# Kernel tuning notes

Measured on AMD Instinct MI355X. Metric: run time of the kernel, lower is better.

## Reference

```python
import jax, jax.numpy as jnp
import numpy as np

B, T, D, A = 8, 256, 512, 512  # hidden dim D must equal attn size A per the TF code


def setup_inputs() -> dict:
    key = jax.random.key(0)
    ks = jax.random.split(key, 12)
    g = lambda k, shp, fan: jax.random.normal(k, shp, jnp.float32) * (1.0 / np.sqrt(fan))
    return {
        "state_outputs": jax.random.normal(ks[0], (B, T, D), jnp.float32),
        "final_state": jax.random.normal(ks[1], (B, D), jnp.float32),
        "intent_v": g(ks[2], (A,), A),
        "W_ih": g(ks[3], (D, A), D), "b_ih": jnp.zeros((A,), jnp.float32),
        "W_ii": g(ks[4], (D, A), D), "b_ii": jnp.zeros((A,), jnp.float32),
        "slot_v": g(ks[5], (A,), A),
        "W_sh": g(ks[6], (D, A), D), "b_sh": jnp.zeros((A,), jnp.float32),
        "W_si": g(ks[7], (D, A), D), "b_si": jnp.zeros((A,), jnp.float32),
    }


def reference(state_outputs, final_state, intent_v, W_ih, b_ih, W_ii, b_ii,
              slot_v, W_sh, b_sh, W_si, b_si):
    # ---- intent attention ----
    ih = jnp.einsum('btd,da->bta', state_outputs, W_ih) + b_ih        # [B,T,A]
    ii = final_state @ W_ii + b_ii                                     # [B,A]
    intent_score = jnp.sum(intent_v * jnp.tanh(ih + ii[:, None, :]), axis=-1)  # [B,T]
    intent_w = jax.nn.softmax(intent_score, axis=-1)
    c_intent = jnp.einsum('bt,btd->bd', intent_w, state_outputs)       # [B,D]

    # ---- slot attention ----
    sh = jnp.einsum('btd,da->bta', state_outputs, W_sh) + b_sh         # keys   [B,T,A]
    si = jnp.einsum('btd,da->bta', state_outputs, W_si) + b_si         # queries[B,T,A]
    # score[b,t,s] over pairs: tanh(sh[b,s] + si[b,t]) . slot_v
    slot_score = jnp.sum(slot_v * jnp.tanh(sh[:, None, :, :] + si[:, :, None, :]), axis=-1)  # [B,T,T]
    slot_w = jax.nn.softmax(slot_score, axis=-1)
    c_slot = jnp.einsum('bts,bsd->btd', slot_w, state_outputs)         # [B,T,D]
    return c_slot, c_intent
```

## Files before the change

kernel.cpp:

```cpp
#include <hip/hip_runtime.h>

#define BB 8
#define TT 256
#define DD 512
#define AA 512

#define PS 2.8853900817779268f
#define LOG2E 1.4426950408889634f

typedef __attribute__((ext_vector_type(8))) short short8;
typedef __attribute__((ext_vector_type(4))) float f32x4;

__device__ __forceinline__ float fast_tanh(float x) {
    float e = __builtin_amdgcn_exp2f(x * PS);
    float r = __builtin_amdgcn_rcpf(1.0f + e);
    return fmaf(-2.0f, r, 1.0f);
}

__device__ __forceinline__ ushort f2bf(float x) {
    uint u = __float_as_uint(x);
    uint r = (u + 0x7fffu + ((u >> 16) & 1u)) >> 16;
    return (ushort)r;
}
__device__ __forceinline__ float bf2f(ushort h) {
    return __uint_as_float(((uint)h) << 16);
}

__global__ __launch_bounds__(256) void prep(const float* __restrict__ SO,
                                            ushort* __restrict__ Ast,
                                            const float* __restrict__ Wsh,
                                            const float* __restrict__ Wsi,
                                            const float* __restrict__ Wih,
                                            ushort* __restrict__ Wt,
                                            const float* __restrict__ fs_g,
                                            const float* __restrict__ Wii,
                                            const float* __restrict__ bii,
                                            float* __restrict__ ii) {
    const int bid = blockIdx.x;
    const int tid = threadIdx.x;
    __shared__ float T[32][33];
    __shared__ float fs[DD];

    if (bid < 16) {
        int b = bid >> 1, half = bid & 1;
        int a = half * 256 + tid;
        fs[tid]       = fs_g[b * DD + tid];
        fs[tid + 256] = fs_g[b * DD + tid + 256];
        __syncthreads();
        float acc = bii[a];
        #pragma unroll 8
        for (int d = 0; d < DD; ++d)
            acc = fmaf(fs[d], Wii[(size_t)d * AA + a], acc);
        ii[b * AA + a] = acc;
    } else if (bid < 784) {
        int lbid = bid - 16;
        int z = lbid >> 8;
        int rem = lbid & 255;
        const float* W = (z == 0) ? Wsh : (z == 1) ? Wsi : Wih;
        int k0 = (rem & 15) * 32, n0 = (rem >> 4) * 32;
        int tx = tid & 31, ty = tid >> 5;
        #pragma unroll
        for (int r = 0; r < 4; ++r) {
            int kl = ty * 4 + r;
            T[kl][tx] = W[(size_t)(k0 + kl) * 512 + n0 + tx];
        }
        __syncthreads();
        size_t nbase = (size_t)z * 512 + n0;
        #pragma unroll
        for (int r = 0; r < 4; ++r) {
            int nl = ty * 4 + r;
            float v = T[tx][nl];
            ushort hi = f2bf(v);
            ushort lo = f2bf(v - bf2f(hi));
            Wt[(nbase + nl) * 1024 + k0 + tx]       = hi;
            Wt[(nbase + nl) * 1024 + 512 + k0 + tx] = lo;
        }
    } else {
        int qid = (bid - 784) * 256 + tid;
        int m = qid >> 7;
        int k4 = (qid & 127) * 4;
        float4 v = *reinterpret_cast<const float4*>(&SO[(size_t)m * 512 + k4]);
        ushort4 hi, lo;
        hi.x = f2bf(v.x); lo.x = f2bf(v.x - bf2f(hi.x));
        hi.y = f2bf(v.y); lo.y = f2bf(v.y - bf2f(hi.y));
        hi.z = f2bf(v.z); lo.z = f2bf(v.z - bf2f(hi.z));
        hi.w = f2bf(v.w); lo.w = f2bf(v.w - bf2f(hi.w));
        *reinterpret_cast<ushort4*>(&Ast[(size_t)m * 1024 + k4])       = hi;
        *reinterpret_cast<ushort4*>(&Ast[(size_t)m * 1024 + 512 + k4]) = lo;
    }
}

__global__ __launch_bounds__(256) void gemm_mfma(
    const ushort* __restrict__ Ast, const ushort* __restrict__ Wt,
    const float* __restrict__ bsh, const float* __restrict__ bsi,
    const float* __restrict__ bih,
    const float* __restrict__ ii, const float* __restrict__ iv,
    float* __restrict__ EhT, float* __restrict__ Es, float* __restrict__ ipart) {
    __shared__ ushort Al[64 * 64];
    __shared__ ushort Bl[64 * 64];
    const int tid = threadIdx.x;
    const int wave = tid >> 6, lane = tid & 63;
    const int wr = wave >> 1, wc = wave & 1;
    const int m0 = blockIdx.x * 64;
    const int by = blockIdx.y;
    const int n0 = by * 64;
    const int r8 = lane >> 3, c8 = lane & 7;
    const int l15 = lane & 15, kb = lane >> 4;

    f32x4 acc[2][2] = {};

    const char* Ab = reinterpret_cast<const char*>(Ast);
    const char* Bb = reinterpret_cast<const char*>(Wt);
    char* AlB = reinterpret_cast<char*>(Al);
    char* BlB = reinterpret_cast<char*>(Bl);

    for (int k0 = 0; k0 < 1536; k0 += 64) {
        int abyte = (k0 < 1024 ? k0 : k0 - 1024) * 2;
        int bbyte = (k0 < 512 ? k0 : k0 - 512) * 2;
        #pragma unroll
        for (int inst = 0; inst < 2; ++inst) {
            int row = wave * 16 + inst * 8 + r8;
            short8 av = *reinterpret_cast<const short8*>(
                Ab + (size_t)(m0 + row) * 2048 + abyte + c8 * 16);
            *reinterpret_cast<short8*>(AlB + row * 128 + ((c8 ^ r8) * 16)) = av;
            short8 bv = *reinterpret_cast<const short8*>(
                Bb + (size_t)(n0 + row) * 2048 + bbyte + c8 * 16);
            *reinterpret_cast<short8*>(BlB + row * 128 + ((c8 ^ r8) * 16)) = bv;
        }
        __syncthreads();
        #pragma unroll
        for (int kk = 0; kk < 2; ++kk) {
            short8 af[2], bf[2];
            #pragma unroll
            for (int i = 0; i < 2; ++i) {
                int ra = wr * 32 + i * 16 + l15;
                int sa = (kk * 4 + kb) ^ (ra & 7);
                af[i] = *reinterpret_cast<const short8*>(AlB + ra * 128 + sa * 16);
                int rb = wc * 32 + i * 16 + l15;
                int sbx = (kk * 4 + kb) ^ (rb & 7);
                bf[i] = *reinterpret_cast<const short8*>(BlB + rb * 128 + sbx * 16);
            }
            #pragma unroll
            for (int i = 0; i < 2; ++i)
                #pragma unroll
                for (int j = 0; j < 2; ++j)
                    acc[i][j] = __builtin_amdgcn_mfma_f32_16x16x32_bf16(
                        af[i], bf[j], acc[i][j], 0, 0, 0);
        }
        __syncthreads();
    }

    const int b = m0 >> 8;
    if (by < 8) {
        #pragma unroll
        for (int i = 0; i < 2; ++i) {
            int t0 = (m0 & 255) + wr * 32 + i * 16 + kb * 4;
            #pragma unroll
            for (int j = 0; j < 2; ++j) {
                int n = n0 + wc * 32 + j * 16 + l15;
                float bbv = bsh[n];
                float4 v;
                v.x = __builtin_amdgcn_exp2f((acc[i][j][0] + bbv) * PS);
                v.y = __builtin_amdgcn_exp2f((acc[i][j][1] + bbv) * PS);
                v.z = __builtin_amdgcn_exp2f((acc[i][j][2] + bbv) * PS);
                v.w = __builtin_amdgcn_exp2f((acc[i][j][3] + bbv) * PS);
                *reinterpret_cast<float4*>(&EhT[((size_t)b * 512 + n) * 256 + t0]) = v;
            }
        }
    } else if (by < 16) {
        #pragma unroll
        for (int i = 0; i < 2; ++i) {
            #pragma unroll
            for (int j = 0; j < 2; ++j) {
                int n = n0 - 512 + wc * 32 + j * 16 + l15;
                float bbv = bsi[n];
                #pragma unroll
                for (int r = 0; r < 4; ++r) {
                    int m = m0 + wr * 32 + i * 16 + kb * 4 + r;
                    Es[(size_t)m * 512 + n] = __builtin_amdgcn_exp2f((acc[i][j][r] + bbv) * PS);
                }
            }
        }
    } else {
        int slot = (by - 16) * 2 + wc;
        #pragma unroll
        for (int i = 0; i < 2; ++i) {
            float p0 = 0.f, p1 = 0.f, p2 = 0.f, p3 = 0.f;
            #pragma unroll
            for (int j = 0; j < 2; ++j) {
                int n = n0 - 1024 + wc * 32 + j * 16 + l15;
                float add = bih[n] + ii[b * 512 + n];
                float w = iv[n];
                p0 = fmaf(w, fast_tanh(acc[i][j][0] + add), p0);
                p1 = fmaf(w, fast_tanh(acc[i][j][1] + add), p1);
                p2 = fmaf(w, fast_tanh(acc[i][j][2] + add), p2);
                p3 = fmaf(w, fast_tanh(acc[i][j][3] + add), p3);
            }
            #pragma unroll
            for (int off = 1; off < 16; off <<= 1) {
                p0 += __shfl_xor(p0, off);
                p1 += __shfl_xor(p1, off);
                p2 += __shfl_xor(p2, off);
                p3 += __shfl_xor(p3, off);
            }
            int mb = m0 + wr * 32 + i * 16 + kb * 4;
            if (l15 == 0) ipart[slot * 2048 + mb + 0] = p0;
            if (l15 == 1) ipart[slot * 2048 + mb + 1] = p1;
            if (l15 == 2) ipart[slot * 2048 + mb + 2] = p2;
            if (l15 == 3) ipart[slot * 2048 + mb + 3] = p3;
        }
    }
}

#define TS 64
#define KS 16
#define LPAD 72

__global__ __launch_bounds__(256) void k0_ii(const float* __restrict__ fs_g,
                                             const float* __restrict__ Wii,
                                             const float* __restrict__ bii,
                                             float* __restrict__ ii) {
    int b = blockIdx.x, tid = threadIdx.x;
    int a = blockIdx.y * 256 + tid;
    __shared__ float fs[DD];
    fs[tid]       = fs_g[b * DD + tid];
    fs[tid + 256] = fs_g[b * DD + tid + 256];
    __syncthreads();
    float acc = bii[a];
    #pragma unroll 8
    for (int d = 0; d < DD; ++d)
        acc = fmaf(fs[d], Wii[(size_t)d * AA + a], acc);
    ii[b * AA + a] = acc;
}

__global__ __launch_bounds__(256) void k1_gemm_old(
    const float* __restrict__ SO,
    const float* __restrict__ Wsh, const float* __restrict__ bsh,
    const float* __restrict__ Wsi, const float* __restrict__ bsi,
    const float* __restrict__ Wih, const float* __restrict__ bih,
    const float* __restrict__ ii, const float* __restrict__ iv,
    float* __restrict__ EhT, float* __restrict__ Es, float* __restrict__ ipart) {
    const int mode = blockIdx.z;
    const float* W;
    const float* bias;
    if (mode == 0)      { W = Wsh; bias = bsh; }
    else if (mode == 1) { W = Wsi; bias = bsi; }
    else                { W = Wih; bias = bih; }

    const int m0 = blockIdx.x * TS;
    const int n0 = blockIdx.y * TS;
    const int tid = threadIdx.x;
    const int tx = tid & 15, ty = tid >> 4;

    __shared__ __align__(16) float As[KS][LPAD];
    __shared__ __align__(16) float Bs[KS][LPAD];
    __shared__ __align__(16) float Cs[TS][LPAD];

    float acc[4][4] = {};
    const int arow = tid >> 2;
    const int akc  = (tid & 3) * 4;
    const int brw  = tid >> 4;
    const int bnc  = (tid & 15) * 4;

    for (int k0 = 0; k0 < DD; k0 += KS) {
        float4 av = *reinterpret_cast<const float4*>(&SO[(m0 + arow) * DD + k0 + akc]);
        As[akc + 0][arow] = av.x;
        As[akc + 1][arow] = av.y;
        As[akc + 2][arow] = av.z;
        As[akc + 3][arow] = av.w;
        float4 bv = *reinterpret_cast<const float4*>(&W[(k0 + brw) * AA + n0 + bnc]);
        *reinterpret_cast<float4*>(&Bs[brw][bnc]) = bv;
        __syncthreads();
        #pragma unroll
        for (int kk = 0; kk < KS; ++kk) {
            float4 a4 = *reinterpret_cast<const float4*>(&As[kk][ty * 4]);
            float4 b4 = *reinterpret_cast<const float4*>(&Bs[kk][tx * 4]);
            float av_[4] = {a4.x, a4.y, a4.z, a4.w};
            float bv_[4] = {b4.x, b4.y, b4.z, b4.w};
            #pragma unroll
            for (int i = 0; i < 4; ++i)
                #pragma unroll
                for (int j = 0; j < 4; ++j)
                    acc[i][j] = fmaf(av_[i], bv_[j], acc[i][j]);
        }
        __syncthreads();
    }

    if (mode == 1) {
        #pragma unroll
        for (int i = 0; i < 4; ++i) {
            int m = m0 + ty * 4 + i;
            float4 v;
            v.x = __builtin_amdgcn_exp2f((acc[i][0] + bias[n0 + tx * 4 + 0]) * PS);
            v.y = __builtin_amdgcn_exp2f((acc[i][1] + bias[n0 + tx * 4 + 1]) * PS);
            v.z = __builtin_amdgcn_exp2f((acc[i][2] + bias[n0 + tx * 4 + 2]) * PS);
            v.w = __builtin_amdgcn_exp2f((acc[i][3] + bias[n0 + tx * 4 + 3]) * PS);
            *reinterpret_cast<float4*>(&Es[(size_t)m * AA + n0 + tx * 4]) = v;
        }
    } else if (mode == 0) {
        #pragma unroll
        for (int i = 0; i < 4; ++i)
            #pragma unroll
            for (int j = 0; j < 4; ++j)
                Cs[tx * 4 + j][ty * 4 + i] =
                    __builtin_amdgcn_exp2f((acc[i][j] + bias[n0 + tx * 4 + j]) * PS);
        __syncthreads();
        int row = tid >> 2, part = tid & 3;
        int bb = m0 >> 8;
        int tstart = (m0 & 255) + part * 16;
        float* dst = &EhT[bb * (AA * TT) + (n0 + row) * TT + tstart];
        #pragma unroll
        for (int q = 0; q < 4; ++q) {
            float4 v = *reinterpret_cast<const float4*>(&Cs[row][part * 16 + q * 4]);
            *reinterpret_cast<float4*>(&dst[q * 4]) = v;
        }
    } else {
        int bb = m0 >> 8;
        #pragma unroll
        for (int i = 0; i < 4; ++i) {
            float p = 0.f;
            #pragma unroll
            for (int j = 0; j < 4; ++j) {
                int n = n0 + tx * 4 + j;
                float x = acc[i][j] + bias[n] + ii[bb * AA + n];
                p = fmaf(iv[n], fast_tanh(x), p);
            }
            Cs[ty * 4 + i][tx] = p;
        }
        __syncthreads();
        if (tid < 64) {
            float s = 0.f;
            #pragma unroll
            for (int k = 0; k < 16; ++k) s += Cs[tid][k];
            ipart[blockIdx.y * 2048 + m0 + tid] = s;
        }
    }
}

__global__ __launch_bounds__(512) void k3_fused(const float* __restrict__ SO,
                                                const float* __restrict__ EhT,
                                                const float* __restrict__ Es,
                                                const float* __restrict__ sv_g,
                                                const float* __restrict__ ipart,
                                                float* __restrict__ out_cslot,
                                                float* __restrict__ out_cint,
                                                int npart) {
    const int bid = blockIdx.x;
    const int tid = threadIdx.x;

    __shared__ float yp[2][4][256];
    __shared__ __align__(16) float wlt[256][4];
    __shared__ float redm[4][4];
    __shared__ float reds[4][4];
    __shared__ float redI[256];
    __shared__ float wlI[256];

    if (bid >= 8) {
        const int sb_ = bid - 8;
        const int b = sb_ & 7;
        const int t0 = (sb_ >> 3) * 4;
        const int s = tid & 255, ah = tid >> 8;
        const int abase = __builtin_amdgcn_readfirstlane(ah << 8);

        const float* e0p = Es + (size_t)(b * 256 + t0 + 0) * 512 + abase;
        const float* e1p = Es + (size_t)(b * 256 + t0 + 1) * 512 + abase;
        const float* e2p = Es + (size_t)(b * 256 + t0 + 2) * 512 + abase;
        const float* e3p = Es + (size_t)(b * 256 + t0 + 3) * 512 + abase;
        const float* svp = sv_g + abase;
        const float* hp  = &EhT[((size_t)b * 512 + abase) * 256 + s];

        float y0 = 0.f, y1 = 0.f, y2 = 0.f, y3 = 0.f;
        for (int a0 = 0; a0 < 256; a0 += 8) {
            float h[8];
            #pragma unroll
            for (int u = 0; u < 8; ++u) h[u] = hp[(a0 + u) * 256];
            #pragma unroll
            for (int u = 0; u < 8; ++u) {
                float v  = svp[a0 + u];
                float hv = h[u];
                y0 = fmaf(v, __builtin_amdgcn_rcpf(fmaf(hv, e0p[a0 + u], 1.0f)), y0);
                y1 = fmaf(v, __builtin_amdgcn_rcpf(fmaf(hv, e1p[a0 + u], 1.0f)), y1);
                y2 = fmaf(v, __builtin_amdgcn_rcpf(fmaf(hv, e2p[a0 + u], 1.0f)), y2);
                y3 = fmaf(v, __builtin_amdgcn_rcpf(fmaf(hv, e3p[a0 + u], 1.0f)), y3);
            }
        }
        yp[ah][0][s] = y0; yp[ah][1][s] = y1; yp[ah][2][s] = y2; yp[ah][3][s] = y3;
        __syncthreads();

        const int wg = (tid >> 6) & 3;
        #pragma unroll
        for (int r = 0; r < 2; ++r) {
            int q = ah * 2 + r;
            float y = yp[0][q][s] + yp[1][q][s];
            float mn = y;
            #pragma unroll
            for (int off = 1; off < 64; off <<= 1)
                mn = fminf(mn, __shfl_xor(mn, off));
            if ((tid & 63) == 0) redm[q][wg] = mn;
            __syncthreads();
            mn = fminf(fminf(redm[q][0], redm[q][1]), fminf(redm[q][2], redm[q][3]));
            float e = __builtin_amdgcn_exp2f(PS * (mn - y));
            float sm = e;
            #pragma unroll
            for (int off = 1; off < 64; off <<= 1)
                sm += __shfl_xor(sm, off);
            if ((tid & 63) == 0) reds[q][wg] = sm;
            __syncthreads();
            sm = (reds[q][0] + reds[q][1]) + (reds[q][2] + reds[q][3]);
            wlt[s][q] = e * __builtin_amdgcn_rcpf(sm);
        }
        __syncthreads();

        const int d = tid;
        const float* sop = &SO[(size_t)b * 256 * 512 + d];
        float c0 = 0.f, c1 = 0.f, c2 = 0.f, c3 = 0.f;
        for (int s0 = 0; s0 < 256; s0 += 4) {
            float so[4];
            #pragma unroll
            for (int u = 0; u < 4; ++u) so[u] = sop[(s0 + u) * 512];
            #pragma unroll
            for (int u = 0; u < 4; ++u) {
                float4 w4 = *reinterpret_cast<const float4*>(&wlt[s0 + u][0]);
                c0 = fmaf(w4.x, so[u], c0);
                c1 = fmaf(w4.y, so[u], c1);
                c2 = fmaf(w4.z, so[u], c2);
                c3 = fmaf(w4.w, so[u], c3);
            }
        }
        float* op = &out_cslot[((size_t)(b * 256 + t0)) * 512 + d];
        op[0] = c0; op[512] = c1; op[1024] = c2; op[1536] = c3;
    } else {
        const int b = bid;
        float sc = 0.f;
        if (tid < 256) {
            for (int nb = 0; nb < npart; ++nb) sc += ipart[nb * 2048 + b * 256 + tid];
            redI[tid] = sc;
        }
        __syncthreads();
        for (int off = 128; off > 0; off >>= 1) {
            if (tid < off) redI[tid] = fmaxf(redI[tid], redI[tid + off]);
            __syncthreads();
        }
        float mx = redI[0];
        __syncthreads();
        float e = 0.f;
        if (tid < 256) { e = __builtin_amdgcn_exp2f((sc - mx) * LOG2E); redI[tid] = e; }
        __syncthreads();
        for (int off = 128; off > 0; off >>= 1) {
            if (tid < off) redI[tid] += redI[tid + off];
            __syncthreads();
        }
        if (tid < 256) wlI[tid] = e * __builtin_amdgcn_rcpf(redI[0]);
        __syncthreads();
        const int d = tid;
        float c = 0.f;
        const float* sop = &SO[(size_t)b * 256 * 512 + d];
        for (int s0 = 0; s0 < 256; s0 += 4) {
            float so[4];
            #pragma unroll
            for (int u = 0; u < 4; ++u) so[u] = sop[(s0 + u) * 512];
            #pragma unroll
            for (int u = 0; u < 4; ++u) c = fmaf(wlI[s0 + u], so[u], c);
        }
        out_cint[(size_t)b * 512 + d] = c;
    }
}

extern "C" void kernel_launch(void* const* d_in, const int* in_sizes, int n_in,
                              void* d_out, int out_size, void* d_ws, size_t ws_size,
                              hipStream_t stream) {
    const float* SO  = (const float*)d_in[0];
    const float* FS  = (const float*)d_in[1];
    const float* IV  = (const float*)d_in[2];
    const float* Wih = (const float*)d_in[3];
    const float* bih = (const float*)d_in[4];
    const float* Wii = (const float*)d_in[5];
    const float* bii = (const float*)d_in[6];
    const float* SV  = (const float*)d_in[7];
    const float* Wsh = (const float*)d_in[8];
    const float* bsh = (const float*)d_in[9];
    const float* Wsi = (const float*)d_in[10];
    const float* bsi = (const float*)d_in[11];

    float* ws    = (float*)d_ws;
    float* EhT   = ws;
    float* Es    = ws + 1048576;
    float* ii    = ws + 2097152;
    float* ipart = ws + 2101248;
    ushort* Ast  = (ushort*)(ws + 2134016);
    ushort* Wt   = (ushort*)(ws + 3182592);
    const size_t NEED = (size_t)3969024 * 4;

    float* out_cslot = (float*)d_out;
    float* out_cint  = out_cslot + BB * TT * DD;

    if (ws_size >= NEED) {
        prep<<<1808, 256, 0, stream>>>(SO, Ast, Wsh, Wsi, Wih, Wt, FS, Wii, bii, ii);
        gemm_mfma<<<dim3(32, 24), 256, 0, stream>>>(Ast, Wt, bsh, bsi, bih, ii, IV,
                                                    EhT, Es, ipart);
        k3_fused<<<520, 512, 0, stream>>>(SO, EhT, Es, SV, ipart, out_cslot, out_cint, 16);
    } else {
        k0_ii<<<dim3(BB, 2), 256, 0, stream>>>(FS, Wii, bii, ii);
        k1_gemm_old<<<dim3(32, 8, 3), 256, 0, stream>>>(SO, Wsh, bsh, Wsi, bsi, Wih, bih,
                                                        ii, IV, EhT, Es, ipart);
        k3_fused<<<520, 512, 0, stream>>>(SO, EhT, Es, SV, ipart, out_cslot, out_cint, 8);
    }
}
```

Baseline: 110.6 us.

## Enlarge MFMA GEMM tiles with double-buffered LDS and widen attention kernel to 1024 threads

Moves the bf16 split GEMM from 64x64 to 128x128 tiles with a K-step of 32. LDS is double-buffered, so the next tile is loaded from global memory while the MFMAs run, and the register accumulators grow to 4x4. The slot-attention kernel now uses 1024 threads, splitting the A reduction four ways and giving each thread two output rows instead of four, to get more parallelism per block. The intent partial count becomes a fixed 8, which matches the new GEMM grid. In exchange, register and LDS pressure rise, the GEMM launches fewer blocks (192) than the GPU has CUs, and the fallback path now also assumes 8 partials.

Result: slower. 126.5 us (+14.4%).

```diff
diff --git a/kernel.cpp b/kernel.cpp
--- a/kernel.cpp
+++ b/kernel.cpp
@@ -96,68 +96,101 @@
     const float* __restrict__ bih,
     const float* __restrict__ ii, const float* __restrict__ iv,
     float* __restrict__ EhT, float* __restrict__ Es, float* __restrict__ ipart) {
-    __shared__ ushort Al[64 * 64];
-    __shared__ ushort Bl[64 * 64];
+    __shared__ __align__(16) ushort Al[2][128 * 32];
+    __shared__ __align__(16) ushort Bl[2][128 * 32];
     const int tid = threadIdx.x;
     const int wave = tid >> 6, lane = tid & 63;
     const int wr = wave >> 1, wc = wave & 1;
-    const int m0 = blockIdx.x * 64;
+    const int m0 = blockIdx.x * 128;
     const int by = blockIdx.y;
-    const int n0 = by * 64;
-    const int r8 = lane >> 3, c8 = lane & 7;
     const int l15 = lane & 15, kb = lane >> 4;
 
-    f32x4 acc[2][2] = {};
+    f32x4 acc[4][4] = {};
 
     const char* Ab = reinterpret_cast<const char*>(Ast);
     const char* Bb = reinterpret_cast<const char*>(Wt);
-    char* AlB = reinterpret_cast<char*>(Al);
-    char* BlB = reinterpret_cast<char*>(Bl);
-
-    for (int k0 = 0; k0 < 1536; k0 += 64) {
-        int abyte = (k0 < 1024 ? k0 : k0 - 1024) * 2;
-        int bbyte = (k0 < 512 ? k0 : k0 - 512) * 2;
-        #pragma unroll
-        for (int inst = 0; inst < 2; ++inst) {
-            int row = wave * 16 + inst * 8 + r8;
-            short8 av = *reinterpret_cast<const short8*>(
-                Ab + (size_t)(m0 + row) * 2048 + abyte + c8 * 16);
-            *reinterpret_cast<short8*>(AlB + row * 128 + ((c8 ^ r8) * 16)) = av;
-            short8 bv = *reinterpret_cast<const short8*>(
-                Bb + (size_t)(n0 + row) * 2048 + bbyte + c8 * 16);
-            *reinterpret_cast<short8*>(BlB + row * 128 + ((c8 ^ r8) * 16)) = bv;
-        }
-        __syncthreads();
-        #pragma unroll
-        for (int kk = 0; kk < 2; ++kk) {
-            short8 af[2], bf[2];
-            #pragma unroll
-            for (int i = 0; i < 2; ++i) {
-                int ra = wr * 32 + i * 16 + l15;
-                int sa = (kk * 4 + kb) ^ (ra & 7);
-                af[i] = *reinterpret_cast<const short8*>(AlB + ra * 128 + sa * 16);
-                int rb = wc * 32 + i * 16 + l15;
-                int sbx = (kk * 4 + kb) ^ (rb & 7);
-                bf[i] = *reinterpret_cast<const short8*>(BlB + rb * 128 + sbx * 16);
-            }
-            #pragma unroll
-            for (int i = 0; i < 2; ++i)
-                #pragma unroll
-                for (int j = 0; j < 2; ++j)
-                    acc[i][j] = __builtin_amdgcn_mfma_f32_16x16x32_bf16(
-                        af[i], bf[j], acc[i][j], 0, 0, 0);
-        }
-        __syncthreads();
+    char* AlB = reinterpret_cast<char*>(&Al[0][0]);
+    char* BlB = reinterpret_cast<char*>(&Bl[0][0]);
+
+    const int srow  = tid >> 1;
+    const int sslot = (tid & 1) * 2;
+    const int swz   = (srow >> 1) & 3;
+    const int lw0 = srow * 64 + ((sslot    ) ^ swz) * 16;
+    const int lw1 = srow * 64 + ((sslot + 1) ^ swz) * 16;
+    const char* agp = Ab + (size_t)(m0 + srow) * 2048 + sslot * 16;
+    const char* bgp = Bb + (size_t)(by * 128 + srow) * 2048 + sslot * 16;
+
+    int aro[4], bro[4];
+    #pragma unroll
+    for (int i = 0; i < 4; ++i) {
+        int ra = wr * 64 + i * 16 + l15;
+        aro[i] = ra * 64 + ((kb ^ ((ra >> 1) & 3)) * 16);
+        int rb = wc * 64 + i * 16 + l15;
+        bro[i] = rb * 64 + ((kb ^ ((rb >> 1) & 3)) * 16);
+    }
+
+    #define ABYTE(k0) (((k0) < 1024 ? (k0) : (k0) - 1024) * 2)
+    #define BBYTE(k0) (((k0) < 512 ? (k0) : (k0) - 512) * 2)
+
+    {
+        short8 a0 = *reinterpret_cast<const short8*>(agp + ABYTE(0));
+        short8 a1 = *reinterpret_cast<const short8*>(agp + ABYTE(0) + 16);
+        short8 b0 = *reinterpret_cast<const short8*>(bgp + BBYTE(0));
+        short8 b1 = *reinterpret_cast<const short8*>(bgp + BBYTE(0) + 16);
+        *reinterpret_cast<short8*>(AlB + lw0) = a0;
+        *reinterpret_cast<short8*>(AlB + lw1) = a1;
+        *reinterpret_cast<short8*>(BlB + lw0) = b0;
+        *reinterpret_cast<short8*>(BlB + lw1) = b1;
+    }
+    __syncthreads();
+
+    int cur = 0;
+    for (int it = 0; it < 48; ++it) {
+        short8 a0, a1, b0, b1;
+        const bool pf = (it + 1 < 48);
+        if (pf) {
+            int k0 = (it + 1) * 32;
+            int ab = ABYTE(k0), bb = BBYTE(k0);
+            a0 = *reinterpret_cast<const short8*>(agp + ab);
+            a1 = *reinterpret_cast<const short8*>(agp + ab + 16);
+            b0 = *reinterpret_cast<const short8*>(bgp + bb);
+            b1 = *reinterpret_cast<const short8*>(bgp + bb + 16);
+        }
+        const char* Ac = AlB + cur * 8192;
+        const char* Bc = BlB + cur * 8192;
+        short8 af[4], bf[4];
+        #pragma unroll
+        for (int i = 0; i < 4; ++i) {
+            af[i] = *reinterpret_cast<const short8*>(Ac + aro[i]);
+            bf[i] = *reinterpret_cast<const short8*>(Bc + bro[i]);
+        }
+        #pragma unroll
+        for (int i = 0; i < 4; ++i)
+            #pragma unroll
+            for (int j = 0; j < 4; ++j)
+                acc[i][j] = __builtin_amdgcn_mfma_f32_16x16x32_bf16(
+                    af[i], bf[j], acc[i][j], 0, 0, 0);
+        if (pf) {
+            char* An = AlB + (cur ^ 1) * 8192;
+            char* Bn = BlB + (cur ^ 1) * 8192;
+            *reinterpret_cast<short8*>(An + lw0) = a0;
+            *reinterpret_cast<short8*>(An + lw1) = a1;
+            *reinterpret_cast<short8*>(Bn + lw0) = b0;
+            *reinterpret_cast<short8*>(Bn + lw1) = b1;
+        }
+        __syncthreads();
+        cur ^= 1;
     }
 
     const int b = m0 >> 8;
-    if (by < 8) {
-        #pragma unroll
-        for (int i = 0; i < 2; ++i) {
-            int t0 = (m0 & 255) + wr * 32 + i * 16 + kb * 4;
-            #pragma unroll
-            for (int j = 0; j < 2; ++j) {
-                int n = n0 + wc * 32 + j * 16 + l15;
+    const int region = by >> 2;
+    if (region == 0) {
+        #pragma unroll
+        for (int i = 0; i < 4; ++i) {
+            int t0 = (m0 & 255) + wr * 64 + i * 16 + kb * 4;
+            #pragma unroll
+            for (int j = 0; j < 4; ++j) {
+                int n = by * 128 + wc * 64 + j * 16 + l15;
                 float bbv = bsh[n];
                 float4 v;
                 v.x = __builtin_amdgcn_exp2f((acc[i][j][0] + bbv) * PS);
@@ -167,28 +200,28 @@
                 *reinterpret_cast<float4*>(&EhT[((size_t)b * 512 + n) * 256 + t0]) = v;
             }
         }
-    } else if (by < 16) {
-        #pragma unroll
-        for (int i = 0; i < 2; ++i) {
-            #pragma unroll
-            for (int j = 0; j < 2; ++j) {
-                int n = n0 - 512 + wc * 32 + j * 16 + l15;
+    } else if (region == 1) {
+        #pragma unroll
+        for (int i = 0; i < 4; ++i) {
+            #pragma unroll
+            for (int j = 0; j < 4; ++j) {
+                int n = (by - 4) * 128 + wc * 64 + j * 16 + l15;
                 float bbv = bsi[n];
                 #pragma unroll
                 for (int r = 0; r < 4; ++r) {
-                    int m = m0 + wr * 32 + i * 16 + kb * 4 + r;
+                    int m = m0 + wr * 64 + i * 16 + kb * 4 + r;
                     Es[(size_t)m * 512 + n] = __builtin_amdgcn_exp2f((acc[i][j][r] + bbv) * PS);
                 }
             }
         }
     } else {
-        int slot = (by - 16) * 2 + wc;
-        #pragma unroll
-        for (int i = 0; i < 2; ++i) {
+        int slot = (by - 8) * 2 + wc;
+        #pragma unroll
+        for (int i = 0; i < 4; ++i) {
             float p0 = 0.f, p1 = 0.f, p2 = 0.f, p3 = 0.f;
             #pragma unroll
-            for (int j = 0; j < 2; ++j) {
-                int n = n0 - 1024 + wc * 32 + j * 16 + l15;
+            for (int j = 0; j < 4; ++j) {
+                int n = (by - 8) * 128 + wc * 64 + j * 16 + l15;
                 float add = bih[n] + ii[b * 512 + n];
                 float w = iv[n];
                 p0 = fmaf(w, fast_tanh(acc[i][j][0] + add), p0);
@@ -203,7 +236,7 @@
                 p2 += __shfl_xor(p2, off);
                 p3 += __shfl_xor(p3, off);
             }
-            int mb = m0 + wr * 32 + i * 16 + kb * 4;
+            int mb = m0 + wr * 64 + i * 16 + kb * 4;
             if (l15 == 0) ipart[slot * 2048 + mb + 0] = p0;
             if (l15 == 1) ipart[slot * 2048 + mb + 1] = p1;
             if (l15 == 2) ipart[slot * 2048 + mb + 2] = p2;
@@ -337,18 +370,17 @@
     }
 }
 
-__global__ __launch_bounds__(512) void k3_fused(const float* __restrict__ SO,
-                                                const float* __restrict__ EhT,
-                                                const float* __restrict__ Es,
-                                                const float* __restrict__ sv_g,
-                                                const float* __restrict__ ipart,
-                                                float* __restrict__ out_cslot,
-                                                float* __restrict__ out_cint,
-                                                int npart) {
+__global__ __launch_bounds__(1024, 8) void k3_fused(const float* __restrict__ SO,
+                                                    const float* __restrict__ EhT,
+                                                    const float* __restrict__ Es,
+                                                    const float* __restrict__ sv_g,
+                                                    const float* __restrict__ ipart,
+                                                    float* __restrict__ out_cslot,
+                                                    float* __restrict__ out_cint) {
     const int bid = blockIdx.x;
     const int tid = threadIdx.x;
 
-    __shared__ float yp[2][4][256];
+    __shared__ float yp[4][4][256];
     __shared__ __align__(16) float wlt[256][4];
     __shared__ float redm[4][4];
     __shared__ float reds[4][4];
@@ -360,7 +392,7 @@
         const int b = sb_ & 7;
         const int t0 = (sb_ >> 3) * 4;
         const int s = tid & 255, ah = tid >> 8;
-        const int abase = __builtin_amdgcn_readfirstlane(ah << 8);
+        const int abase = ah << 7;
 
         const float* e0p = Es + (size_t)(b * 256 + t0 + 0) * 512 + abase;
         const float* e1p = Es + (size_t)(b * 256 + t0 + 1) * 512 + abase;
@@ -370,7 +402,7 @@
         const float* hp  = &EhT[((size_t)b * 512 + abase) * 256 + s];
 
         float y0 = 0.f, y1 = 0.f, y2 = 0.f, y3 = 0.f;
-        for (int a0 = 0; a0 < 256; a0 += 8) {
+        for (int a0 = 0; a0 < 128; a0 += 8) {
             float h[8];
             #pragma unroll
             for (int u = 0; u < 8; ++u) h[u] = hp[(a0 + u) * 256];
@@ -387,53 +419,49 @@
         yp[ah][0][s] = y0; yp[ah][1][s] = y1; yp[ah][2][s] = y2; yp[ah][3][s] = y3;
         __syncthreads();
 
+        const int g = ah;
         const int wg = (tid >> 6) & 3;
-        #pragma unroll
-        for (int r = 0; r < 2; ++r) {
-            int q = ah * 2 + r;
-            float y = yp[0][q][s] + yp[1][q][s];
-            float mn = y;
-            #pragma unroll
-            for (int off = 1; off < 64; off <<= 1)
-                mn = fminf(mn, __shfl_xor(mn, off));
-            if ((tid & 63) == 0) redm[q][wg] = mn;
-            __syncthreads();
-            mn = fminf(fminf(redm[q][0], redm[q][1]), fminf(redm[q][2], redm[q][3]));
-            float e = __builtin_amdgcn_exp2f(PS * (mn - y));
-            float sm = e;
-            #pragma unroll
-            for (int off = 1; off < 64; off <<= 1)
-                sm += __shfl_xor(sm, off);
-            if ((tid & 63) == 0) reds[q][wg] = sm;
-            __syncthreads();
-            sm = (reds[q][0] + reds[q][1]) + (reds[q][2] + reds[q][3]);
-            wlt[s][q] = e * __builtin_amdgcn_rcpf(sm);
-        }
-        __syncthreads();
-
-        const int d = tid;
+        float y = (yp[0][g][s] + yp[1][g][s]) + (yp[2][g][s] + yp[3][g][s]);
+        float mn = y;
+        #pragma unroll
+        for (int off = 1; off < 64; off <<= 1)
+            mn = fminf(mn, __shfl_xor(mn, off));
+        if ((tid & 63) == 0) redm[g][wg] = mn;
+        __syncthreads();
+        mn = fminf(fminf(redm[g][0], redm[g][1]), fminf(redm[g][2], redm[g][3]));
+        float e = __builtin_amdgcn_exp2f(PS * (mn - y));
+        float sm = e;
+        #pragma unroll
+        for (int off = 1; off < 64; off <<= 1)
+            sm += __shfl_xor(sm, off);
+        if ((tid & 63) == 0) reds[g][wg] = sm;
+        __syncthreads();
+        sm = (reds[g][0] + reds[g][1]) + (reds[g][2] + reds[g][3]);
+        wlt[s][g] = e * __builtin_amdgcn_rcpf(sm);
+        __syncthreads();
+
+        const int d = tid & 511, th = tid >> 9;
         const float* sop = &SO[(size_t)b * 256 * 512 + d];
-        float c0 = 0.f, c1 = 0.f, c2 = 0.f, c3 = 0.f;
+        float c0 = 0.f, c1 = 0.f;
         for (int s0 = 0; s0 < 256; s0 += 4) {
             float so[4];
             #pragma unroll
             for (int u = 0; u < 4; ++u) so[u] = sop[(s0 + u) * 512];
             #pragma unroll
             for (int u = 0; u < 4; ++u) {
-                float4 w4 = *reinterpret_cast<const float4*>(&wlt[s0 + u][0]);
-                c0 = fmaf(w4.x, so[u], c0);
-                c1 = fmaf(w4.y, so[u], c1);
-                c2 = fmaf(w4.z, so[u], c2);
-                c3 = fmaf(w4.w, so[u], c3);
-            }
-        }
-        float* op = &out_cslot[((size_t)(b * 256 + t0)) * 512 + d];
-        op[0] = c0; op[512] = c1; op[1024] = c2; op[1536] = c3;
+                float2 w2 = *reinterpret_cast<const float2*>(&wlt[s0 + u][2 * th]);
+                c0 = fmaf(w2.x, so[u], c0);
+                c1 = fmaf(w2.y, so[u], c1);
+            }
+        }
+        float* op = &out_cslot[((size_t)(b * 256 + t0 + 2 * th)) * 512 + d];
+        op[0] = c0; op[512] = c1;
     } else {
         const int b = bid;
         float sc = 0.f;
         if (tid < 256) {
-            for (int nb = 0; nb < npart; ++nb) sc += ipart[nb * 2048 + b * 256 + tid];
+            #pragma unroll
+            for (int nb = 0; nb < 8; ++nb) sc += ipart[nb * 2048 + b * 256 + tid];
             redI[tid] = sc;
         }
         __syncthreads();
@@ -452,17 +480,19 @@
         }
         if (tid < 256) wlI[tid] = e * __builtin_amdgcn_rcpf(redI[0]);
         __syncthreads();
-        const int d = tid;
-        float c = 0.f;
-        const float* sop = &SO[(size_t)b * 256 * 512 + d];
-        for (int s0 = 0; s0 < 256; s0 += 4) {
-            float so[4];
-            #pragma unroll
-            for (int u = 0; u < 4; ++u) so[u] = sop[(s0 + u) * 512];
-            #pragma unroll
-            for (int u = 0; u < 4; ++u) c = fmaf(wlI[s0 + u], so[u], c);
-        }
-        out_cint[(size_t)b * 512 + d] = c;
+        if (tid < 512) {
+            const int d = tid;
+            float c = 0.f;
+            const float* sop = &SO[(size_t)b * 256 * 512 + d];
+            for (int s0 = 0; s0 < 256; s0 += 4) {
+                float so[4];
+                #pragma unroll
+                for (int u = 0; u < 4; ++u) so[u] = sop[(s0 + u) * 512];
+                #pragma unroll
+                for (int u = 0; u < 4; ++u) c = fmaf(wlI[s0 + u], so[u], c);
+            }
+            out_cint[(size_t)b * 512 + d] = c;
+        }
     }
 }
 
@@ -496,13 +526,13 @@
 
     if (ws_size >= NEED) {
         prep<<<1808, 256, 0, stream>>>(SO, Ast, Wsh, Wsi, Wih, Wt, FS, Wii, bii, ii);
-        gemm_mfma<<<dim3(32, 24), 256, 0, stream>>>(Ast, Wt, bsh, bsi, bih, ii, IV,
+        gemm_mfma<<<dim3(16, 12), 256, 0, stream>>>(Ast, Wt, bsh, bsi, bih, ii, IV,
                                                     EhT, Es, ipart);
-        k3_fused<<<520, 512, 0, stream>>>(SO, EhT, Es, SV, ipart, out_cslot, out_cint, 16);
+        k3_fused<<<520, 1024, 0, stream>>>(SO, EhT, Es, SV, ipart, out_cslot, out_cint);
     } else {
         k0_ii<<<dim3(BB, 2), 256, 0, stream>>>(FS, Wii, bii, ii);
         k1_gemm_old<<<dim3(32, 8, 3), 256, 0, stream>>>(SO, Wsh, bsh, Wsi, bsi, Wih, bih,
                                                         ii, IV, EhT, Es, ipart);
-        k3_fused<<<520, 512, 0, stream>>>(SO, EhT, Es, SV, ipart, out_cslot, out_cint, 8);
-    }
-}
+        k3_fused<<<520, 1024, 0, stream>>>(SO, EhT, Es, SV, ipart, out_cslot, out_cint);
+    }
+}
```
